# Kernel optimization log

Hardware: AMD Instinct MI355X
Metric: run time of the kernel (lower is better)

## Reference

```python
import jax, jax.numpy as jnp
import numpy as np

EPS = 1e-5
NUM_CRYSTALS = 64


def _bn(x2d, g, b):
    # torch BatchNorm1d in training mode: biased batch stats, affine
    m = x2d.mean(0)
    v = x2d.var(0)
    return g * (x2d - m) * jax.lax.rsqrt(v + EPS) + b


def _improved_conv(x, e, idx, p):
    (fcW, fcb, g1, b1, g2, b2, eW, eb, ge, be, W3, b3, g3, b3b) = p
    N, M = idx.shape
    A = x.shape[1]
    Bf = e.shape[2]
    xn = x[idx]  # (N, M, A) gathered neighbor atom features
    tot = jnp.concatenate([jnp.broadcast_to(x[:, None, :], (N, M, A)), xn, e], axis=2)  # (N,M,2A+B)
    # 2-body gated message
    h = jnp.einsum('nmf,of->nmo', tot, fcW) + fcb
    h = _bn(h.reshape(-1, 2 * A), g1, b1).reshape(N, M, 2 * A)
    two_body = jnp.sum(jax.nn.sigmoid(h[..., :A]) * jax.nn.softplus(h[..., A:]), axis=1)
    # explicit edge update
    he = jnp.einsum('nmf,of->nmo', tot, eW) + eb
    he = _bn(he.reshape(-1, 2 * Bf), ge, be).reshape(N, M, 2 * Bf)
    e_out = e + jax.nn.sigmoid(he[..., :Bf]) * jax.nn.softplus(he[..., Bf:])
    # 3-body: split W3 by concat blocks [x_i, x_j, x_l, e_ij, e_il] so the
    # (N,M,M,3A+2B) concat is never materialized; only (N,M,M,2A) is formed.
    Wa, Wj, Wl, Wij, Wil = jnp.split(W3, [A, 2 * A, 3 * A, 3 * A + Bf], axis=1)
    h3 = ((x @ Wa.T)[:, None, None, :]
          + (xn @ Wj.T)[:, :, None, :]
          + (xn @ Wl.T)[:, None, :, :]
          + (e @ Wij.T)[:, :, None, :]
          + (e @ Wil.T)[:, None, :, :]
          + b3)  # (N, M, M, 2A)
    h3 = _bn(h3.reshape(-1, 2 * A), g3, b3b).reshape(N, M, M, 2 * A)
    three_body = jnp.sum(jax.nn.sigmoid(h3[..., :A]) * jax.nn.softplus(h3[..., A:]), axis=(1, 2))
    total = _bn(two_body + three_body, g2, b2)
    return jax.nn.softplus(x + total), e_out


def setup_inputs() -> dict:
    key = jax.random.key(0)
    ks = jax.random.split(key, 12)
    N, M, OF, A, BF, H, NC = 2000, 12, 92, 64, 41, 128, 3
    f = lambda k, s: jax.random.normal(k, s, dtype=jnp.float32) * 0.05
    z = lambda s: jnp.zeros(s, jnp.float32)
    o = lambda s: jnp.ones(s, jnp.float32)
    return {
        'atom_fea': jax.random.normal(ks[0], (N, OF), dtype=jnp.float32),
        'nbr_fea': jax.random.normal(ks[1], (N, M, BF), dtype=jnp.float32),
        'nbr_fea_idx': jax.random.randint(ks[2], (N, M), 0, N),
        'site_seg': jnp.sort(jax.random.randint(ks[3], (N,), 0, NUM_CRYSTALS)),
        'emb_W': f(ks[4], (A, OF)), 'emb_b': z((A,)),
        'fcW': f(ks[5], (NC, 2 * A, 2 * A + BF)), 'fcb': z((NC, 2 * A)),
        'bn1_g': o((NC, 2 * A)), 'bn1_b': z((NC, 2 * A)),
        'bn2_g': o((NC, A)), 'bn2_b': z((NC, A)),
        'eW': f(ks[6], (NC, 2 * BF, 2 * A + BF)), 'eb': z((NC, 2 * BF)),
        'bne_g': o((NC, 2 * BF)), 'bne_b': z((NC, 2 * BF)),
        'W3': f(ks[7], (NC, 2 * A, 3 * A + 2 * BF)), 'b3': z((NC, 2 * A)),
        'bn3_g': o((NC, 2 * A)), 'bn3_b': z((NC, 2 * A)),
        'fc1W': f(ks[8], (H, A)), 'fc1b': z((H,)),
        'outW': f(ks[9], (1, H)), 'outb': z((1,)),
    }


def reference(atom_fea, nbr_fea, nbr_fea_idx, site_seg, emb_W, emb_b,
              fcW, fcb, bn1_g, bn1_b, bn2_g, bn2_b, eW, eb, bne_g, bne_b,
              W3, b3, bn3_g, bn3_b, fc1W, fc1b, outW, outb):
    x = atom_fea @ emb_W.T + emb_b  # embedding1 (orbital=False)
    e = nbr_fea
    n_conv = fcW.shape[0]
    for i in range(n_conv):  # small fixed layer loop
        p = (fcW[i], fcb[i], bn1_g[i], bn1_b[i], bn2_g[i], bn2_b[i],
             eW[i], eb[i], bne_g[i], bne_b[i], W3[i], b3[i], bn3_g[i], bn3_b[i])
        x, e = _improved_conv(x, e, nbr_fea_idx, p)
    x = jax.nn.softplus(jax.nn.softplus(x) @ fc1W.T + fc1b)  # conv_to_fc1
    # per-crystal mean pooling over site segments
    N = x.shape[0]
    sums = jax.ops.segment_sum(x, site_seg, num_segments=NUM_CRYSTALS)
    counts = jax.ops.segment_sum(jnp.ones((N, 1), x.dtype), site_seg, num_segments=NUM_CRYSTALS)
    pooled = sums / jnp.maximum(counts, 1.0)
    return pooled @ outW.T + outb  # (NUM_CRYSTALS, 1)
```

## Files before the change

### kernel.cpp

```cpp
#include <hip/hip_runtime.h>
#include <hip/hip_bf16.h>

#define N_ATOM 2000
#define MNBR   12
#define OFEA   92
#define AF     64
#define BFEA   41
#define K1     169
#define O1     128
#define OE     82
#define K3     274
#define NM     24000
#define NCONV  3
#define HID    128
#define NCRY   64
#define EPS_BN 1e-5f

#define LDA_T  192
#define LDH    512
#define LDSW   88
#define LDE    48

typedef __bf16 bf16x8 __attribute__((ext_vector_type(8)));
typedef float  f32x4  __attribute__((ext_vector_type(4)));

__device__ __forceinline__ float sigmoidf_(float x){
    return __builtin_amdgcn_rcpf(1.f + __expf(-x));
}
__device__ __forceinline__ float softplusf_(float x){
    return fmaxf(x,0.f) + __logf(1.f + __expf(-fabsf(x)));
}

__device__ __forceinline__ uint4 pack_bf16_8(const float* v){
    __hip_bfloat16 o[8];
    #pragma unroll
    for (int j=0;j<8;j++) o[j] = __float2bfloat16(v[j]);
    return *(const uint4*)o;
}

__global__ __launch_bounds__(256, 3)
void gemm_fused(const float* __restrict__ X,
                const float* __restrict__ E48,
                const int*   __restrict__ idx,
                const __hip_bfloat16* __restrict__ W,
                const float* __restrict__ bias,
                float* __restrict__ REST,
                float* __restrict__ STL,
                float* __restrict__ SPA,
                float* __restrict__ SQA)
{
    __shared__ unsigned short As[128][LDSW];
    __shared__ unsigned short Ws[128][LDSW];
    __shared__ float cs1[128];
    __shared__ float cs2[128];
    __shared__ float spa[12][128];

    const int tid  = threadIdx.x;
    const int row0 = blockIdx.x * 128;
    const int col0 = blockIdx.y * 128;
    const int w    = tid >> 6;
    const int l    = tid & 63;
    const int wm   = w >> 1, wn = w & 1;
    const int lrow = l & 15;
    const int quad = l >> 4;

    if (tid < 128){ cs1[tid] = 0.f; cs2[tid] = 0.f; }
    for (int ii = tid; ii < 12*128; ii += 256) spa[ii>>7][ii&127] = 0.f;

    f32x4 acc[4][4];
    #pragma unroll
    for (int i=0;i<4;i++)
        #pragma unroll
        for (int j=0;j<4;j++) acc[i][j] = (f32x4){0.f,0.f,0.f,0.f};

    #pragma unroll
    for (int it = 0; it < 3; ++it){
        const int k0 = it * 64;
        if (it) __syncthreads();
        #pragma unroll
        for (int j = 0; j < 4; ++j){
            int e  = tid + j*256;
            int r  = e >> 3;
            int kk = (e & 7) << 3;
            int grow = row0 + r;
            float v[8];
            #pragma unroll
            for (int q2=0;q2<8;q2++) v[q2] = 0.f;
            if (grow < NM){
                if (it == 2){
                    if (kk < LDE){
                        const float* s = E48 + (size_t)grow*LDE + kk;
                        float4 a0 = *(const float4*)s;
                        float4 a1 = *(const float4*)(s+4);
                        v[0]=a0.x; v[1]=a0.y; v[2]=a0.z; v[3]=a0.w;
                        v[4]=a1.x; v[5]=a1.y; v[6]=a1.z; v[7]=a1.w;
                    }
                } else {
                    const float* s = (it == 0)
                        ? X + (size_t)((unsigned)grow/12u)*AF + kk
                        : X + (size_t)idx[grow]*AF + kk;
                    float4 a0 = *(const float4*)s;
                    float4 a1 = *(const float4*)(s+4);
                    v[0]=a0.x; v[1]=a0.y; v[2]=a0.z; v[3]=a0.w;
                    v[4]=a1.x; v[5]=a1.y; v[6]=a1.z; v[7]=a1.w;
                }
            }
            *(uint4*)(&As[r][kk]) = pack_bf16_8(v);
            uint4 vw = *(const uint4*)(W + (size_t)(col0 + r)*LDA_T + k0 + kk);
            *(uint4*)(&Ws[r][kk]) = vw;
        }
        __syncthreads();
        #pragma unroll
        for (int ks = 0; ks < 2; ++ks){
            int koff = ks*32 + quad*8;
            bf16x8 a_[4], b_[4];
            #pragma unroll
            for (int mi=0;mi<4;mi++)
                a_[mi] = *(const bf16x8*)(&As[wm*64 + mi*16 + lrow][koff]);
            #pragma unroll
            for (int ni=0;ni<4;ni++)
                b_[ni] = *(const bf16x8*)(&Ws[wn*64 + ni*16 + lrow][koff]);
            #pragma unroll
            for (int mi=0;mi<4;mi++)
                #pragma unroll
                for (int ni=0;ni<4;ni++)
                    acc[mi][ni] = __builtin_amdgcn_mfma_f32_16x16x32_bf16(
                        a_[mi], b_[ni], acc[mi][ni], 0, 0, 0);
        }
    }

    const bool isPQ = (col0 >= 256);
    const int atomBase = (unsigned)row0 / 12u;
    int rbase_[4], n0_[4], sp_[4];
    #pragma unroll
    for (int mi=0;mi<4;mi++){
        rbase_[mi] = row0 + wm*64 + mi*16 + quad*4;
        int n0 = (int)((unsigned)rbase_[mi] / 12u);
        n0_[mi] = n0;
        sp_[mi] = 12 - (rbase_[mi] - n0*12);
    }

    #pragma unroll
    for (int ni=0;ni<4;ni++){
        const int cl  = wn*64 + ni*16 + lrow;
        const int col = col0 + cl;
        const float bv = bias[col];
        float s1 = 0.f, s2 = 0.f;
        #pragma unroll
        for (int mi=0;mi<4;mi++){
            const int rbase = rbase_[mi];
            float run0 = 0.f, run1 = 0.f;
            #pragma unroll
            for (int reg=0;reg<4;reg++){
                int grow = rbase + reg;
                if (grow < NM){
                    float vv = acc[mi][ni][reg] + bv;
                    if (col0 != 128 || col < 210)
                        REST[(size_t)grow*LDH + col] = vv;
                    s1 += vv; s2 += vv*vv;
                    if (isPQ){
                        if (reg < sp_[mi]) run0 += vv; else run1 += vv;
                    }
                }
            }
            if (isPQ){
                if (run0 != 0.f) atomicAdd(&spa[n0_[mi]     - atomBase][cl], run0);
                if (run1 != 0.f) atomicAdd(&spa[n0_[mi] + 1 - atomBase][cl], run1);
            }
        }
        if (isPQ){
            atomicAdd(&cs2[cl], s2);
        } else {
            atomicAdd(&cs1[cl], s1);
            atomicAdd(&cs2[cl], s2);
        }
    }
    __syncthreads();
    if (!isPQ){
        if (tid < 128){
            atomicAdd(&STL[col0 + tid],       cs1[tid]);
            atomicAdd(&STL[256 + col0 + tid], cs2[tid]);
        }
    } else {
        if (tid < 128)
            atomicAdd(&STL[(col0 == 256 ? 896 : 1024) + tid], cs2[tid]);
        float* SPQd = (col0 == 256) ? SPA : SQA;
        for (int ii = tid; ii < 12*128; ii += 256){
            int ai = ii >> 7, c2 = ii & 127;
            int na = atomBase + ai;
            float val = spa[ai][c2];
            if (val != 0.f && na < N_ATOM)
                atomicAdd(&SPQd[(size_t)na*128 + c2], val);
        }
    }
}

__global__ __launch_bounds__(256)
void bn3_pre(const float* __restrict__ SPA, const float* __restrict__ SQA,
             float* __restrict__ STL)
{
    const int c    = threadIdx.x & 127;
    const int half = threadIdx.x >> 7;
    float s1 = 0.f, sx = 0.f;
    for (int n = blockIdx.x*2 + half; n < N_ATOM; n += 64){
        float p = SPA[(size_t)n*128 + c];
        float q = SQA[(size_t)n*128 + c];
        s1 += p + q;
        sx += p * q;
    }
    atomicAdd(&STL[512 + c], 12.f*s1);
    atomicAdd(&STL[640 + c], 2.f*sx);
}

#define BM 64
#define BN 128
#define BK 32
template<int EPI, int SPIN>
__global__ __launch_bounds__(256)
void gemm_tn(const float* __restrict__ T, int ldt, int R,
             const float* __restrict__ W, int ldw, int K, int O,
             const float* __restrict__ bias,
             float* __restrict__ C, int ldc)
{
    __shared__ float Ts[BM][BK+1];
    __shared__ float Ws2[BN][BK+1];
    const int tid = threadIdx.x;
    const int row0 = blockIdx.x * BM;
    const int tx = tid % 16;
    const int ty = tid / 16;
    float acc[4][8];
    #pragma unroll
    for (int i=0;i<4;i++)
        #pragma unroll
        for (int j=0;j<8;j++) acc[i][j]=0.f;

    for (int k0 = 0; k0 < K; k0 += BK) {
        #pragma unroll
        for (int i=0;i<(BM*BK)/256;i++){
            int e = tid + i*256;
            int r = e / BK, k = e % BK;
            int gr = row0 + r, gk = k0 + k;
            float v = 0.f;
            if (gr < R && gk < K){
                v = T[(size_t)gr*ldt + gk];
                if (SPIN) v = softplusf_(v);
            }
            Ts[r][k] = v;
        }
        #pragma unroll
        for (int i=0;i<(BN*BK)/256;i++){
            int e = tid + i*256;
            int r = e / BK, k = e % BK;
            int gk = k0 + k;
            Ws2[r][k] = (r < O && gk < K) ? W[(size_t)r*ldw + gk] : 0.f;
        }
        __syncthreads();
        #pragma unroll
        for (int k=0;k<BK;k++){
            float a_[4], b_[8];
            #pragma unroll
            for (int i=0;i<4;i++) a_[i] = Ts[ty*4+i][k];
            #pragma unroll
            for (int j=0;j<8;j++) b_[j] = Ws2[tx + j*16][k];
            #pragma unroll
            for (int i=0;i<4;i++)
                #pragma unroll
                for (int j=0;j<8;j++)
                    acc[i][j] += a_[i]*b_[j];
        }
        __syncthreads();
    }
    #pragma unroll
    for (int i=0;i<4;i++){
        int gr = row0 + ty*4 + i;
        if (gr >= R) continue;
        #pragma unroll
        for (int j=0;j<8;j++){
            int gc = tx + j*16;
            if (gc >= O) continue;
            float v = acc[i][j] + (bias ? bias[gc] : 0.f);
            if (EPI==1) v = softplusf_(v);
            C[(size_t)gr*ldc + gc] = v;
        }
    }
}

__global__ void pack_all(const float* __restrict__ fcW, const float* __restrict__ eW,
                         const float* __restrict__ W3, const float* __restrict__ fcb,
                         const float* __restrict__ eb, const float* __restrict__ b3,
                         __hip_bfloat16* __restrict__ WALL, float* __restrict__ BIAS)
{
    int i = blockIdx.x*blockDim.x + threadIdx.x;
    const int nW = NCONV*512*LDA_T;
    if (i < nW){
        int l = i/(512*LDA_T), rem = i%(512*LDA_T);
        int c = rem/LDA_T, k = rem%LDA_T;
        float v = 0.f;
        if (c < O1){
            if (k < K1) v = fcW[((size_t)l*O1 + c)*K1 + k];
        } else if (c < O1+OE){
            if (k < K1) v = eW[((size_t)l*OE + (c-O1))*K1 + k];
        } else if (c >= 256 && c < 384){
            int o = c - 256;
            const float* W3l = W3 + (size_t)l*O1*K3;
            if (k < AF)                        v = 0.5f * W3l[(size_t)o*K3 + k];
            else if (k < 2*AF)                 v = W3l[(size_t)o*K3 + k];
            else if (k < K1)                   v = W3l[(size_t)o*K3 + 192 + (k-128)];
        } else if (c >= 384){
            int o = c - 384;
            const float* W3l = W3 + (size_t)l*O1*K3;
            if (k < AF)                        v = 0.5f * W3l[(size_t)o*K3 + k];
            else if (k < 2*AF)                 v = W3l[(size_t)o*K3 + k + AF];
            else if (k < K1)                   v = W3l[(size_t)o*K3 + 233 + (k-128)];
        }
        WALL[i] = __float2bfloat16(v);
    } else if (i < nW + NCONV*512){
        int m = i - nW;
        int l = m/512, c = m%512;
        float v = 0.f;
        if (c < O1)         v = fcb[l*O1 + c];
        else if (c < O1+OE) v = eb[l*OE + (c-O1)];
        else if (c >= 256)  v = 0.5f * b3[l*O1 + ((c-256)&127)];
        BIAS[m] = v;
    }
}

__global__ void e_init(const float* __restrict__ nbr, float* __restrict__ E48)
{
    int i = blockIdx.x*blockDim.x + threadIdx.x;
    if (i >= NM*LDE) return;
    int r = i / LDE, k = i % LDE;
    E48[i] = (k < BFEA) ? nbr[(size_t)r*BFEA + k] : 0.f;
}

__global__ void bn_fin_all(const float* __restrict__ STL,
                           const float* __restrict__ g1, const float* __restrict__ b1,
                           const float* __restrict__ ge, const float* __restrict__ be,
                           const float* __restrict__ g3, const float* __restrict__ b3b,
                           float* __restrict__ SC)
{
    int c = threadIdx.x;
    const float* S1A = STL;
    const float* S2A = STL + 256;
    const float* S13 = STL + 512;
    const float* S23 = STL + 640;
    const float* S2P = STL + 896;
    const float* S2Q = STL + 1024;
    if (c < O1+OE){
        float mean = S1A[c]*(1.f/NM);
        float var  = fmaxf(S2A[c]*(1.f/NM) - mean*mean, 0.f);
        float gg = (c < O1) ? g1[c] : ge[c-O1];
        float bb = (c < O1) ? b1[c] : be[c-O1];
        float sc = gg * rsqrtf(var + EPS_BN);
        SC[c] = sc; SC[256+c] = bb - sc*mean;
    }
    if (c < O1){
        float inv  = 1.f/((float)NM*MNBR);
        float mean = S13[c]*inv;
        float ex2  = (S23[c] + 12.f*(S2P[c] + S2Q[c]))*inv;
        float var  = fmaxf(ex2 - mean*mean, 0.f);
        float sc = g3[c] * rsqrtf(var + EPS_BN);
        SC[512+c] = sc; SC[640+c] = b3b[c] - sc*mean;
    }
}

__global__ __launch_bounds__(128)
void consumer_k(const float* __restrict__ REST, const float* __restrict__ SC,
                float* __restrict__ TB, float* __restrict__ E48)
{
    __shared__ float red[128];
    const int n = blockIdx.x;
    const int t = threadIdx.x;
    const int a = t & 63;
    const int g = t >> 6;
    const float* base = REST + (size_t)n*MNBR*LDH;

    float sha = SC[a],      tha = SC[256+a];
    float shb = SC[64+a],   thb = SC[256+64+a];
    float s3lo = SC[512+a], s3hi = SC[512+64+a];
    float t3lo = SC[640+a], t3hi = SC[640+64+a];

    float Qa[MNBR], Qb[MNBR];
    #pragma unroll
    for (int m=0;m<MNBR;m++){
        const float* row = base + (size_t)m*LDH;
        Qa[m] = s3lo*row[384+a];
        Qb[m] = s3hi*row[448+a];
    }
    float acc = 0.f;
    #pragma unroll
    for (int j=0;j<6;j++){
        const float* row = base + (size_t)(g*6+j)*LDH;
        acc += sigmoidf_(sha*row[a]+tha) * softplusf_(shb*row[64+a]+thb);
        float ua = s3lo*row[256+a] + t3lo;
        float ub = s3hi*row[320+a] + t3hi;
        #pragma unroll
        for (int l2=0;l2<MNBR;l2++)
            acc += sigmoidf_(ua + Qa[l2]) * softplusf_(ub + Qb[l2]);
    }
    red[t] = acc;
    __syncthreads();
    if (g == 0)
        TB[(size_t)n*AF + a] = red[a] + red[64+a];
    for (int idx = t; idx < MNBR*BFEA; idx += 128){
        int m = idx / BFEA, b = idx % BFEA;
        const float* row = base + (size_t)m*LDH;
        float u = SC[O1+b]*row[O1+b]   + SC[256+O1+b];
        float v = SC[169+b]*row[169+b] + SC[256+169+b];
        E48[((size_t)n*MNBR + m)*LDE + b] += sigmoidf_(u) * softplusf_(v);
    }
}

__global__ __launch_bounds__(64)
void tb_stats_k(const float* __restrict__ TB,
                float* __restrict__ S1, float* __restrict__ S2)
{
    int t = threadIdx.x;
    float s1 = 0.f, s2 = 0.f;
    for (int r = blockIdx.x; r < N_ATOM; r += gridDim.x){
        float v = TB[(size_t)r*AF + t];
        s1 += v; s2 += v*v;
    }
    atomicAdd(&S1[t], s1);
    atomicAdd(&S2[t], s2);
}

__global__ void x_update_k(float* __restrict__ X, const float* __restrict__ TB,
                           const float* __restrict__ S12, const float* __restrict__ S22,
                           const float* __restrict__ g2, const float* __restrict__ b2,
                           int total)
{
    int i = blockIdx.x*blockDim.x + threadIdx.x;
    if (i >= total) return;
    int a = i & (AF-1);
    float mean = S12[a]*(1.f/N_ATOM);
    float var  = fmaxf(S22[a]*(1.f/N_ATOM) - mean*mean, 0.f);
    float sc = g2[a]*rsqrtf(var + EPS_BN);
    X[i] = softplusf_(X[i] + sc*TB[i] + (b2[a] - sc*mean));
}

__global__ __launch_bounds__(128)
void pool_out_k(const float* __restrict__ Z, const int* __restrict__ seg,
                const float* __restrict__ outW, const float* __restrict__ outb,
                float* __restrict__ out)
{
    __shared__ float red[128];
    const int c = blockIdx.x;
    const int h = threadIdx.x;
    int l0, l1;
    {
        int l=0, r=N_ATOM;
        while (l<r){ int m=(l+r)>>1; if (seg[m] < c) l=m+1; else r=m; }
        l0 = l;
        l=l0; r=N_ATOM;
        while (l<r){ int m=(l+r)>>1; if (seg[m] < c+1) l=m+1; else r=m; }
        l1 = l;
    }
    float s = 0.f;
    for (int n = l0; n < l1; ++n) s += Z[(size_t)n*HID + h];
    float cnt = fmaxf((float)(l1-l0), 1.f);
    red[h] = (s/cnt) * outW[h];
    __syncthreads();
    for (int off=64; off>0; off>>=1){
        if (h < off) red[h] += red[h+off];
        __syncthreads();
    }
    if (h == 0) out[c] = red[0] + outb[0];
}

extern "C" void kernel_launch(void* const* d_in, const int* in_sizes, int n_in,
                              void* d_out, int out_size, void* d_ws, size_t ws_size,
                              hipStream_t stream)
{
    const float* atom_fea = (const float*)d_in[0];
    const float* nbr_fea  = (const float*)d_in[1];
    const int*   nbr_idx  = (const int*)d_in[2];
    const int*   site_seg = (const int*)d_in[3];
    const float* emb_W = (const float*)d_in[4];
    const float* emb_b = (const float*)d_in[5];
    const float* fcW   = (const float*)d_in[6];
    const float* fcb   = (const float*)d_in[7];
    const float* bn1_g = (const float*)d_in[8];
    const float* bn1_b = (const float*)d_in[9];
    const float* bn2_g = (const float*)d_in[10];
    const float* bn2_b = (const float*)d_in[11];
    const float* eW    = (const float*)d_in[12];
    const float* eb    = (const float*)d_in[13];
    const float* bne_g = (const float*)d_in[14];
    const float* bne_b = (const float*)d_in[15];
    const float* W3    = (const float*)d_in[16];
    const float* b3    = (const float*)d_in[17];
    const float* bn3_g = (const float*)d_in[18];
    const float* bn3_b = (const float*)d_in[19];
    const float* fc1W  = (const float*)d_in[20];
    const float* fc1b  = (const float*)d_in[21];
    const float* outW  = (const float*)d_in[22];
    const float* outb  = (const float*)d_in[23];

    float* ws   = (float*)d_ws;
    float* X    = ws;
    float* E48  = ws + 128000;
    float* REST = ws + 1280000;
    float* TB   = ws + 13568000;
    float* Z    = ws + 13696000;
    float* ST   = ws + 13952000;
    float* SC   = ws + 13958144;
    float* SPQ  = ws + 13959168;
    __hip_bfloat16* WALL = (__hip_bfloat16*)(ws + 15495168);
    float* BIAS = ws + 15642624;

    {
        int tot = NCONV*512*LDA_T + NCONV*512;
        pack_all<<<(tot+255)/256, 256, 0, stream>>>(fcW, eW, W3, fcb, eb, b3, WALL, BIAS);
    }
    hipMemsetAsync(ST, 0, (size_t)(6144 + 1024 + 1536000) * sizeof(float), stream);
    gemm_tn<0,0><<<(N_ATOM+BM-1)/BM, 256, 0, stream>>>(atom_fea, OFEA, N_ATOM,
                                                       emb_W, OFEA, OFEA, AF, emb_b, X, AF);
    e_init<<<(NM*LDE+255)/256, 256, 0, stream>>>(nbr_fea, E48);

    for (int i = 0; i < NCONV; i++){
        const float* g1 = bn1_g + i*O1, *b1 = bn1_b + i*O1;
        const float* g2 = bn2_g + i*AF, *b2 = bn2_b + i*AF;
        const float* ge = bne_g + i*OE, *be = bne_b + i*OE;
        const float* g3 = bn3_g + i*O1, *b3b = bn3_b + i*O1;
        float* STL = ST + i*2048;
        float* SPA = SPQ + (size_t)i*512000;
        float* SQA = SPA + 256000;
        float *S12 = STL+768, *S22 = STL+832;

        {
            dim3 g((NM+127)/128, 4);
            gemm_fused<<<g, 256, 0, stream>>>(X, E48, nbr_idx,
                                              WALL + (size_t)i*512*LDA_T,
                                              BIAS + i*512, REST, STL, SPA, SQA);
        }
        bn3_pre<<<32, 256, 0, stream>>>(SPA, SQA, STL);
        bn_fin_all<<<1, 256, 0, stream>>>(STL, g1, b1, ge, be, g3, b3b, SC);
        consumer_k<<<N_ATOM, 128, 0, stream>>>(REST, SC, TB, E48);
        tb_stats_k<<<128, 64, 0, stream>>>(TB, S12, S22);
        x_update_k<<<(N_ATOM*AF+255)/256, 256, 0, stream>>>(X, TB, S12, S22, g2, b2,
                                                            N_ATOM*AF);
    }

    gemm_tn<1,1><<<(N_ATOM+BM-1)/BM, 256, 0, stream>>>(X, AF, N_ATOM, fc1W, AF, AF, HID,
                                                       fc1b, Z, HID);
    pool_out_k<<<NCRY, 128, 0, stream>>>(Z, site_seg, outW, outb, (float*)d_out);
}
```

Baseline: 405.3 us.

## Fuse each conv layer into one persistent kernel with grid barriers

Replaces the per-layer chain of gemm_fused, bn3_pre, bn_fin_all, consumer_k, tb_stats_k and x_update_k with a single persistent kernel of 250 blocks of 512 threads. Each block owns 8 atoms (96 edge rows) and all 512 output columns, and keeps the GEMM results in registers and LDS instead of writing the large REST buffer to global memory. Batch-norm statistics are combined across blocks through global atomics and two software grid barriers. This removes heavy global traffic and several launches, but it relies on all 250 blocks being co-resident, and it recomputes the 3-body pair terms per block with less parallelism per atom.

```diff
diff --git a/kernel.cpp b/kernel.cpp
--- a/kernel.cpp
+++ b/kernel.cpp
@@ -9,7 +9,6 @@
 #define K1     169
 #define O1     128
 #define OE     82
-#define K3     274
 #define NM     24000
 #define NCONV  3
 #define HID    128
@@ -17,199 +16,316 @@
 #define EPS_BN 1e-5f
 
 #define LDA_T  192
-#define LDH    512
 #define LDSW   88
 #define LDE    48
+#define LDP    260
+#define TPB    512
+#define NBLK   250
 
 typedef __bf16 bf16x8 __attribute__((ext_vector_type(8)));
 typedef float  f32x4  __attribute__((ext_vector_type(4)));
 
+#define AS_OFF    0
+#define WS_OFF    16896
+#define HPQ_OFF   16896
+#define BL_OFF    116736
+#define SCT_OFF   118784
+#define SHT_OFF   119808
+#define SC3_OFF   120832
+#define SH3_OFF   121344
+#define S13_OFF   121856
+#define S23_OFF   122368
+#define TBL_OFF   122880
+#define DYN_LDS   124928
+
 __device__ __forceinline__ float sigmoidf_(float x){
     return __builtin_amdgcn_rcpf(1.f + __expf(-x));
 }
 __device__ __forceinline__ float softplusf_(float x){
     return fmaxf(x,0.f) + __logf(1.f + __expf(-fabsf(x)));
 }
-
 __device__ __forceinline__ uint4 pack_bf16_8(const float* v){
     __hip_bfloat16 o[8];
     #pragma unroll
     for (int j=0;j<8;j++) o[j] = __float2bfloat16(v[j]);
     return *(const uint4*)o;
 }
-
-__global__ __launch_bounds__(256, 3)
-void gemm_fused(const float* __restrict__ X,
-                const float* __restrict__ E48,
-                const int*   __restrict__ idx,
-                const __hip_bfloat16* __restrict__ W,
-                const float* __restrict__ bias,
-                float* __restrict__ REST,
-                float* __restrict__ STL,
-                float* __restrict__ SPA,
-                float* __restrict__ SQA)
+__device__ __forceinline__ float aloadf(const float* p){
+    return __hip_atomic_load((float*)p, __ATOMIC_RELAXED, __HIP_MEMORY_SCOPE_AGENT);
+}
+
+__device__ __forceinline__ void gridbar(unsigned* bar, unsigned target){
+    __syncthreads();
+    if (threadIdx.x == 0){
+        unsigned* cnt = bar;
+        unsigned* gen = bar + 1;
+        unsigned g = __hip_atomic_load(gen, __ATOMIC_RELAXED, __HIP_MEMORY_SCOPE_AGENT);
+        unsigned a = __hip_atomic_fetch_add(cnt, 1u, __ATOMIC_ACQ_REL, __HIP_MEMORY_SCOPE_AGENT);
+        if (a + 1 == target){
+            __hip_atomic_store(cnt, 0u, __ATOMIC_RELAXED, __HIP_MEMORY_SCOPE_AGENT);
+            __hip_atomic_fetch_add(gen, 1u, __ATOMIC_RELEASE, __HIP_MEMORY_SCOPE_AGENT);
+        } else {
+            while (__hip_atomic_load(gen, __ATOMIC_ACQUIRE, __HIP_MEMORY_SCOPE_AGENT) == g)
+                __builtin_amdgcn_s_sleep(4);
+        }
+    }
+    __syncthreads();
+}
+
+__global__ __launch_bounds__(TPB, 2)
+void mega_k(float* __restrict__ X, float* __restrict__ E48,
+            const int* __restrict__ idx,
+            const __hip_bfloat16* __restrict__ W, const float* __restrict__ bias,
+            float* __restrict__ STL, unsigned* __restrict__ bar,
+            const float* __restrict__ g1, const float* __restrict__ b1,
+            const float* __restrict__ ge, const float* __restrict__ be,
+            const float* __restrict__ g3, const float* __restrict__ b3b,
+            const float* __restrict__ g2, const float* __restrict__ b2)
 {
-    __shared__ unsigned short As[128][LDSW];
-    __shared__ unsigned short Ws[128][LDSW];
-    __shared__ float cs1[128];
-    __shared__ float cs2[128];
-    __shared__ float spa[12][128];
-
-    const int tid  = threadIdx.x;
-    const int row0 = blockIdx.x * 128;
-    const int col0 = blockIdx.y * 128;
+    extern __shared__ char smem[];
+    unsigned short (*As)[LDSW] = (unsigned short(*)[LDSW])(smem + AS_OFF);
+    unsigned short (*Ws)[LDSW] = (unsigned short(*)[LDSW])(smem + WS_OFF);
+    float (*HPQ)[LDP] = (float(*)[LDP])(smem + HPQ_OFF);
+    float* bL   = (float*)(smem + BL_OFF);
+    float* scT  = (float*)(smem + SCT_OFF);
+    float* shT  = (float*)(smem + SHT_OFF);
+    float* sc3  = (float*)(smem + SC3_OFF);
+    float* sh3  = (float*)(smem + SH3_OFF);
+    float* s13L = (float*)(smem + S13_OFF);
+    float* s23L = (float*)(smem + S23_OFF);
+    float* tbL  = (float*)(smem + TBL_OFF);
+
+    const int tid = threadIdx.x;
     const int w    = tid >> 6;
     const int l    = tid & 63;
-    const int wm   = w >> 1, wn = w & 1;
+    const int wm   = w >> 2;
+    const int cg   = w & 3;
     const int lrow = l & 15;
     const int quad = l >> 4;
-
-    if (tid < 128){ cs1[tid] = 0.f; cs2[tid] = 0.f; }
-    for (int ii = tid; ii < 12*128; ii += 256) spa[ii>>7][ii&127] = 0.f;
-
-    f32x4 acc[4][4];
+    const int row0 = blockIdx.x * 96;
+    const int atomBase = blockIdx.x * 8;
+
+    bL[tid] = bias[tid];
+    if (tid < 128){ s13L[tid] = 0.f; s23L[tid] = 0.f; }
+
+    f32x4 acc[3][8];
     #pragma unroll
-    for (int i=0;i<4;i++)
-        #pragma unroll
-        for (int j=0;j<4;j++) acc[i][j] = (f32x4){0.f,0.f,0.f,0.f};
+    for (int i=0;i<3;i++)
+        #pragma unroll
+        for (int j=0;j<8;j++) acc[i][j] = (f32x4){0.f,0.f,0.f,0.f};
 
     #pragma unroll
     for (int it = 0; it < 3; ++it){
         const int k0 = it * 64;
-        if (it) __syncthreads();
-        #pragma unroll
-        for (int j = 0; j < 4; ++j){
-            int e  = tid + j*256;
+        __syncthreads();
+        for (int e = tid; e < 768; e += TPB){
             int r  = e >> 3;
             int kk = (e & 7) << 3;
             int grow = row0 + r;
             float v[8];
             #pragma unroll
             for (int q2=0;q2<8;q2++) v[q2] = 0.f;
-            if (grow < NM){
-                if (it == 2){
-                    if (kk < LDE){
-                        const float* s = E48 + (size_t)grow*LDE + kk;
-                        float4 a0 = *(const float4*)s;
-                        float4 a1 = *(const float4*)(s+4);
-                        v[0]=a0.x; v[1]=a0.y; v[2]=a0.z; v[3]=a0.w;
-                        v[4]=a1.x; v[5]=a1.y; v[6]=a1.z; v[7]=a1.w;
-                    }
-                } else {
-                    const float* s = (it == 0)
-                        ? X + (size_t)((unsigned)grow/12u)*AF + kk
-                        : X + (size_t)idx[grow]*AF + kk;
+            if (it == 2){
+                if (kk < LDE){
+                    const float* s = E48 + (size_t)grow*LDE + kk;
                     float4 a0 = *(const float4*)s;
                     float4 a1 = *(const float4*)(s+4);
                     v[0]=a0.x; v[1]=a0.y; v[2]=a0.z; v[3]=a0.w;
                     v[4]=a1.x; v[5]=a1.y; v[6]=a1.z; v[7]=a1.w;
                 }
+            } else {
+                const float* s = (it == 0)
+                    ? X + (size_t)(atomBase + r/12)*AF + kk
+                    : X + (size_t)idx[grow]*AF + kk;
+                float4 a0 = *(const float4*)s;
+                float4 a1 = *(const float4*)(s+4);
+                v[0]=a0.x; v[1]=a0.y; v[2]=a0.z; v[3]=a0.w;
+                v[4]=a1.x; v[5]=a1.y; v[6]=a1.z; v[7]=a1.w;
             }
             *(uint4*)(&As[r][kk]) = pack_bf16_8(v);
-            uint4 vw = *(const uint4*)(W + (size_t)(col0 + r)*LDA_T + k0 + kk);
-            *(uint4*)(&Ws[r][kk]) = vw;
+        }
+        for (int e = tid; e < 4096; e += TPB){
+            int r  = e >> 3;
+            int kk = (e & 7) << 3;
+            *(uint4*)(&Ws[r][kk]) = *(const uint4*)(W + (size_t)r*LDA_T + k0 + kk);
         }
         __syncthreads();
         #pragma unroll
         for (int ks = 0; ks < 2; ++ks){
             int koff = ks*32 + quad*8;
-            bf16x8 a_[4], b_[4];
-            #pragma unroll
-            for (int mi=0;mi<4;mi++)
-                a_[mi] = *(const bf16x8*)(&As[wm*64 + mi*16 + lrow][koff]);
-            #pragma unroll
-            for (int ni=0;ni<4;ni++)
-                b_[ni] = *(const bf16x8*)(&Ws[wn*64 + ni*16 + lrow][koff]);
-            #pragma unroll
-            for (int mi=0;mi<4;mi++)
+            bf16x8 a_[3], b_[8];
+            #pragma unroll
+            for (int mi=0;mi<3;mi++)
+                a_[mi] = *(const bf16x8*)(&As[wm*48 + mi*16 + lrow][koff]);
+            #pragma unroll
+            for (int ni=0;ni<8;ni++)
+                b_[ni] = *(const bf16x8*)(&Ws[cg*128 + ni*16 + lrow][koff]);
+            #pragma unroll
+            for (int mi=0;mi<3;mi++)
                 #pragma unroll
-                for (int ni=0;ni<4;ni++)
+                for (int ni=0;ni<8;ni++)
                     acc[mi][ni] = __builtin_amdgcn_mfma_f32_16x16x32_bf16(
                         a_[mi], b_[ni], acc[mi][ni], 0, 0, 0);
         }
     }
 
-    const bool isPQ = (col0 >= 256);
-    const int atomBase = (unsigned)row0 / 12u;
-    int rbase_[4], n0_[4], sp_[4];
-    #pragma unroll
-    for (int mi=0;mi<4;mi++){
-        rbase_[mi] = row0 + wm*64 + mi*16 + quad*4;
-        int n0 = (int)((unsigned)rbase_[mi] / 12u);
-        n0_[mi] = n0;
-        sp_[mi] = 12 - (rbase_[mi] - n0*12);
-    }
-
-    #pragma unroll
-    for (int ni=0;ni<4;ni++){
-        const int cl  = wn*64 + ni*16 + lrow;
-        const int col = col0 + cl;
-        const float bv = bias[col];
-        float s1 = 0.f, s2 = 0.f;
-        #pragma unroll
-        for (int mi=0;mi<4;mi++){
-            const int rbase = rbase_[mi];
-            float run0 = 0.f, run1 = 0.f;
-            #pragma unroll
-            for (int reg=0;reg<4;reg++){
-                int grow = rbase + reg;
-                if (grow < NM){
-                    float vv = acc[mi][ni][reg] + bv;
-                    if (col0 != 128 || col < 210)
-                        REST[(size_t)grow*LDH + col] = vv;
-                    s1 += vv; s2 += vv*vv;
-                    if (isPQ){
-                        if (reg < sp_[mi]) run0 += vv; else run1 += vv;
-                    }
+    __syncthreads();
+    if (cg < 2){
+        #pragma unroll
+        for (int mi=0;mi<3;mi++)
+            #pragma unroll
+            for (int ni=0;ni<8;ni++){
+                int cl = cg*128 + ni*16 + lrow;
+                float bv = bL[cl];
+                #pragma unroll
+                for (int reg=0;reg<4;reg++){
+                    int rl = wm*48 + mi*16 + quad*4 + reg;
+                    HPQ[rl][cl] = acc[mi][ni][reg] + bv;
                 }
             }
-            if (isPQ){
-                if (run0 != 0.f) atomicAdd(&spa[n0_[mi]     - atomBase][cl], run0);
-                if (run1 != 0.f) atomicAdd(&spa[n0_[mi] + 1 - atomBase][cl], run1);
+    }
+    __syncthreads();
+    if (tid < 256){
+        float s1 = 0.f, s2 = 0.f;
+        for (int r = 0; r < 96; ++r){
+            float v = HPQ[r][tid];
+            s1 += v; s2 += v*v;
+        }
+        atomicAdd(&STL[tid],       s1);
+        atomicAdd(&STL[256 + tid], s2);
+    }
+    __syncthreads();
+    if (cg >= 2){
+        #pragma unroll
+        for (int mi=0;mi<3;mi++)
+            #pragma unroll
+            for (int ni=0;ni<8;ni++){
+                int cl = (cg-2)*128 + ni*16 + lrow;
+                float bv = bL[256 + cl];
+                #pragma unroll
+                for (int reg=0;reg<4;reg++){
+                    int rl = wm*48 + mi*16 + quad*4 + reg;
+                    HPQ[rl][cl] = acc[mi][ni][reg] + bv;
+                }
             }
-        }
-        if (isPQ){
-            atomicAdd(&cs2[cl], s2);
-        } else {
-            atomicAdd(&cs1[cl], s1);
-            atomicAdd(&cs2[cl], s2);
-        }
-    }
-    __syncthreads();
-    if (!isPQ){
-        if (tid < 128){
-            atomicAdd(&STL[col0 + tid],       cs1[tid]);
-            atomicAdd(&STL[256 + col0 + tid], cs2[tid]);
-        }
-    } else {
-        if (tid < 128)
-            atomicAdd(&STL[(col0 == 256 ? 896 : 1024) + tid], cs2[tid]);
-        float* SPQd = (col0 == 256) ? SPA : SQA;
-        for (int ii = tid; ii < 12*128; ii += 256){
-            int ai = ii >> 7, c2 = ii & 127;
-            int na = atomBase + ai;
-            float val = spa[ai][c2];
-            if (val != 0.f && na < N_ATOM)
-                atomicAdd(&SPQd[(size_t)na*128 + c2], val);
-        }
-    }
-}
-
-__global__ __launch_bounds__(256)
-void bn3_pre(const float* __restrict__ SPA, const float* __restrict__ SQA,
-             float* __restrict__ STL)
-{
-    const int c    = threadIdx.x & 127;
-    const int half = threadIdx.x >> 7;
-    float s1 = 0.f, sx = 0.f;
-    for (int n = blockIdx.x*2 + half; n < N_ATOM; n += 64){
-        float p = SPA[(size_t)n*128 + c];
-        float q = SQA[(size_t)n*128 + c];
-        s1 += p + q;
-        sx += p * q;
-    }
-    atomicAdd(&STL[512 + c], 12.f*s1);
-    atomicAdd(&STL[640 + c], 2.f*sx);
+    }
+    __syncthreads();
+    for (int item = tid; item < 1024; item += TPB){
+        int n = item >> 7, c = item & 127;
+        int r0 = n * MNBR;
+        float sp=0.f, spp=0.f, sq=0.f, sqq=0.f;
+        #pragma unroll
+        for (int m=0;m<MNBR;m++){
+            float p = HPQ[r0+m][c];
+            float q = HPQ[r0+m][128+c];
+            sp += p; spp += p*p; sq += q; sqq += q*q;
+        }
+        atomicAdd(&s13L[c], 12.f*(sp+sq));
+        atomicAdd(&s23L[c], 12.f*(spp+sqq) + 2.f*sp*sq);
+    }
+    __syncthreads();
+    if (tid < 128){
+        atomicAdd(&STL[512 + tid], s13L[tid]);
+        atomicAdd(&STL[640 + tid], s23L[tid]);
+    }
+
+    gridbar(bar, NBLK);
+
+    if (tid < 256){
+        int c = tid;
+        if (c < O1+OE){
+            float mean = aloadf(&STL[c]) * (1.f/NM);
+            float var  = fmaxf(aloadf(&STL[256+c])*(1.f/NM) - mean*mean, 0.f);
+            float gg = (c < O1) ? g1[c] : ge[c-O1];
+            float bb = (c < O1) ? b1[c] : be[c-O1];
+            float sc = gg * rsqrtf(var + EPS_BN);
+            scT[c] = sc; shT[c] = bb - sc*mean;
+        }
+    } else if (tid < 384){
+        int c = tid - 256;
+        float inv  = 1.f/((float)NM*MNBR);
+        float mean = aloadf(&STL[512+c]) * inv;
+        float var  = fmaxf(aloadf(&STL[640+c])*inv - mean*mean, 0.f);
+        float sc = g3[c] * rsqrtf(var + EPS_BN);
+        sc3[c] = sc; sh3[c] = b3b[c] - sc*mean;
+    }
+    __syncthreads();
+
+    const int r0a = w * MNBR;
+    float acc3 = 0.f;
+    {
+        float s3lo = sc3[l],    t3lo = sh3[l];
+        float s3hi = sc3[64+l], t3hi = sh3[64+l];
+        float Qa[MNBR], Qb[MNBR], ua[MNBR], ub[MNBR];
+        #pragma unroll
+        for (int m=0;m<MNBR;m++){
+            Qa[m] = s3lo*HPQ[r0a+m][128+l];
+            Qb[m] = s3hi*HPQ[r0a+m][192+l];
+            ua[m] = s3lo*HPQ[r0a+m][l]      + t3lo;
+            ub[m] = s3hi*HPQ[r0a+m][64+l]   + t3hi;
+        }
+        #pragma unroll
+        for (int m=0;m<MNBR;m++)
+            #pragma unroll
+            for (int l2=0;l2<MNBR;l2++)
+                acc3 += sigmoidf_(ua[m]+Qa[l2]) * softplusf_(ub[m]+Qb[l2]);
+    }
+    __syncthreads();
+    if (cg < 2){
+        #pragma unroll
+        for (int mi=0;mi<3;mi++)
+            #pragma unroll
+            for (int ni=0;ni<8;ni++){
+                int cl = cg*128 + ni*16 + lrow;
+                float bv = bL[cl];
+                #pragma unroll
+                for (int reg=0;reg<4;reg++){
+                    int rl = wm*48 + mi*16 + quad*4 + reg;
+                    HPQ[rl][cl] = acc[mi][ni][reg] + bv;
+                }
+            }
+    }
+    __syncthreads();
+    {
+        float sha = scT[l],    tha = shT[l];
+        float shb = scT[64+l], thb = shT[64+l];
+        float acc2 = 0.f;
+        #pragma unroll
+        for (int m=0;m<MNBR;m++)
+            acc2 += sigmoidf_(sha*HPQ[r0a+m][l]+tha) * softplusf_(shb*HPQ[r0a+m][64+l]+thb);
+        tbL[tid] = acc2 + acc3;
+    }
+    for (int item = tid; item < 8*MNBR*BFEA; item += TPB){
+        int n = item / (MNBR*BFEA);
+        int rem = item % (MNBR*BFEA);
+        int m = rem / BFEA, b = rem % BFEA;
+        const float* hr = HPQ[n*MNBR + m];
+        float u = scT[O1+b]*hr[O1+b]   + shT[O1+b];
+        float vv = scT[169+b]*hr[169+b] + shT[169+b];
+        E48[((size_t)(atomBase+n)*MNBR + m)*LDE + b] += sigmoidf_(u) * softplusf_(vv);
+    }
+    __syncthreads();
+    if (tid < 64){
+        float s1 = 0.f, s2 = 0.f;
+        #pragma unroll
+        for (int n=0;n<8;n++){
+            float v = tbL[n*64 + tid];
+            s1 += v; s2 += v*v;
+        }
+        atomicAdd(&STL[768 + tid], s1);
+        atomicAdd(&STL[832 + tid], s2);
+    }
+
+    gridbar(bar, NBLK);
+
+    {
+        int n = tid >> 6, a2 = tid & 63;
+        float mean = aloadf(&STL[768+a2]) * (1.f/N_ATOM);
+        float var  = fmaxf(aloadf(&STL[832+a2])*(1.f/N_ATOM) - mean*mean, 0.f);
+        float sc = g2[a2]*rsqrtf(var + EPS_BN);
+        size_t gx = (size_t)(atomBase+n)*AF + a2;
+        X[gx] = softplusf_(X[gx] + sc*tbL[tid] + (b2[a2] - sc*mean));
+    }
 }
 
 #define BM 64
@@ -293,34 +409,34 @@
     int i = blockIdx.x*blockDim.x + threadIdx.x;
     const int nW = NCONV*512*LDA_T;
     if (i < nW){
-        int l = i/(512*LDA_T), rem = i%(512*LDA_T);
+        int ll = i/(512*LDA_T), rem = i%(512*LDA_T);
         int c = rem/LDA_T, k = rem%LDA_T;
         float v = 0.f;
         if (c < O1){
-            if (k < K1) v = fcW[((size_t)l*O1 + c)*K1 + k];
+            if (k < K1) v = fcW[((size_t)ll*O1 + c)*K1 + k];
         } else if (c < O1+OE){
-            if (k < K1) v = eW[((size_t)l*OE + (c-O1))*K1 + k];
+            if (k < K1) v = eW[((size_t)ll*OE + (c-O1))*K1 + k];
         } else if (c >= 256 && c < 384){
             int o = c - 256;
-            const float* W3l = W3 + (size_t)l*O1*K3;
-            if (k < AF)                        v = 0.5f * W3l[(size_t)o*K3 + k];
-            else if (k < 2*AF)                 v = W3l[(size_t)o*K3 + k];
-            else if (k < K1)                   v = W3l[(size_t)o*K3 + 192 + (k-128)];
+            const float* W3l = W3 + (size_t)ll*O1*274;
+            if (k < AF)                        v = 0.5f * W3l[(size_t)o*274 + k];
+            else if (k < 2*AF)                 v = W3l[(size_t)o*274 + k];
+            else if (k < K1)                   v = W3l[(size_t)o*274 + 192 + (k-128)];
         } else if (c >= 384){
             int o = c - 384;
-            const float* W3l = W3 + (size_t)l*O1*K3;
-            if (k < AF)                        v = 0.5f * W3l[(size_t)o*K3 + k];
-            else if (k < 2*AF)                 v = W3l[(size_t)o*K3 + k + AF];
-            else if (k < K1)                   v = W3l[(size_t)o*K3 + 233 + (k-128)];
+            const float* W3l = W3 + (size_t)ll*O1*274;
+            if (k < AF)                        v = 0.5f * W3l[(size_t)o*274 + k];
+            else if (k < 2*AF)                 v = W3l[(size_t)o*274 + k + AF];
+            else if (k < K1)                   v = W3l[(size_t)o*274 + 233 + (k-128)];
         }
         WALL[i] = __float2bfloat16(v);
     } else if (i < nW + NCONV*512){
         int m = i - nW;
-        int l = m/512, c = m%512;
+        int ll = m/512, c = m%512;
         float v = 0.f;
-        if (c < O1)         v = fcb[l*O1 + c];
-        else if (c < O1+OE) v = eb[l*OE + (c-O1)];
-        else if (c >= 256)  v = 0.5f * b3[l*O1 + ((c-256)&127)];
+        if (c < O1)         v = fcb[ll*O1 + c];
+        else if (c < O1+OE) v = eb[ll*OE + (c-O1)];
+        else if (c >= 256)  v = 0.5f * b3[ll*O1 + ((c-256)&127)];
         BIAS[m] = v;
     }
 }
@@ -331,112 +447,6 @@
     if (i >= NM*LDE) return;
     int r = i / LDE, k = i % LDE;
     E48[i] = (k < BFEA) ? nbr[(size_t)r*BFEA + k] : 0.f;
-}
-
-__global__ void bn_fin_all(const float* __restrict__ STL,
-                           const float* __restrict__ g1, const float* __restrict__ b1,
-                           const float* __restrict__ ge, const float* __restrict__ be,
-                           const float* __restrict__ g3, const float* __restrict__ b3b,
-                           float* __restrict__ SC)
-{
-    int c = threadIdx.x;
-    const float* S1A = STL;
-    const float* S2A = STL + 256;
-    const float* S13 = STL + 512;
-    const float* S23 = STL + 640;
-    const float* S2P = STL + 896;
-    const float* S2Q = STL + 1024;
-    if (c < O1+OE){
-        float mean = S1A[c]*(1.f/NM);
-        float var  = fmaxf(S2A[c]*(1.f/NM) - mean*mean, 0.f);
-        float gg = (c < O1) ? g1[c] : ge[c-O1];
-        float bb = (c < O1) ? b1[c] : be[c-O1];
-        float sc = gg * rsqrtf(var + EPS_BN);
-        SC[c] = sc; SC[256+c] = bb - sc*mean;
-    }
-    if (c < O1){
-        float inv  = 1.f/((float)NM*MNBR);
-        float mean = S13[c]*inv;
-        float ex2  = (S23[c] + 12.f*(S2P[c] + S2Q[c]))*inv;
-        float var  = fmaxf(ex2 - mean*mean, 0.f);
-        float sc = g3[c] * rsqrtf(var + EPS_BN);
-        SC[512+c] = sc; SC[640+c] = b3b[c] - sc*mean;
-    }
-}
-
-__global__ __launch_bounds__(128)
-void consumer_k(const float* __restrict__ REST, const float* __restrict__ SC,
-                float* __restrict__ TB, float* __restrict__ E48)
-{
-    __shared__ float red[128];
-    const int n = blockIdx.x;
-    const int t = threadIdx.x;
-    const int a = t & 63;
-    const int g = t >> 6;
-    const float* base = REST + (size_t)n*MNBR*LDH;
-
-    float sha = SC[a],      tha = SC[256+a];
-    float shb = SC[64+a],   thb = SC[256+64+a];
-    float s3lo = SC[512+a], s3hi = SC[512+64+a];
-    float t3lo = SC[640+a], t3hi = SC[640+64+a];
-
-    float Qa[MNBR], Qb[MNBR];
-    #pragma unroll
-    for (int m=0;m<MNBR;m++){
-        const float* row = base + (size_t)m*LDH;
-        Qa[m] = s3lo*row[384+a];
-        Qb[m] = s3hi*row[448+a];
-    }
-    float acc = 0.f;
-    #pragma unroll
-    for (int j=0;j<6;j++){
-        const float* row = base + (size_t)(g*6+j)*LDH;
-        acc += sigmoidf_(sha*row[a]+tha) * softplusf_(shb*row[64+a]+thb);
-        float ua = s3lo*row[256+a] + t3lo;
-        float ub = s3hi*row[320+a] + t3hi;
-        #pragma unroll
-        for (int l2=0;l2<MNBR;l2++)
-            acc += sigmoidf_(ua + Qa[l2]) * softplusf_(ub + Qb[l2]);
-    }
-    red[t] = acc;
-    __syncthreads();
-    if (g == 0)
-        TB[(size_t)n*AF + a] = red[a] + red[64+a];
-    for (int idx = t; idx < MNBR*BFEA; idx += 128){
-        int m = idx / BFEA, b = idx % BFEA;
-        const float* row = base + (size_t)m*LDH;
-        float u = SC[O1+b]*row[O1+b]   + SC[256+O1+b];
-        float v = SC[169+b]*row[169+b] + SC[256+169+b];
-        E48[((size_t)n*MNBR + m)*LDE + b] += sigmoidf_(u) * softplusf_(v);
-    }
-}
-
-__global__ __launch_bounds__(64)
-void tb_stats_k(const float* __restrict__ TB,
-                float* __restrict__ S1, float* __restrict__ S2)
-{
-    int t = threadIdx.x;
-    float s1 = 0.f, s2 = 0.f;
-    for (int r = blockIdx.x; r < N_ATOM; r += gridDim.x){
-        float v = TB[(size_t)r*AF + t];
-        s1 += v; s2 += v*v;
-    }
-    atomicAdd(&S1[t], s1);
-    atomicAdd(&S2[t], s2);
-}
-
-__global__ void x_update_k(float* __restrict__ X, const float* __restrict__ TB,
-                           const float* __restrict__ S12, const float* __restrict__ S22,
-                           const float* __restrict__ g2, const float* __restrict__ b2,
-                           int total)
-{
-    int i = blockIdx.x*blockDim.x + threadIdx.x;
-    if (i >= total) return;
-    int a = i & (AF-1);
-    float mean = S12[a]*(1.f/N_ATOM);
-    float var  = fmaxf(S22[a]*(1.f/N_ATOM) - mean*mean, 0.f);
-    float sc = g2[a]*rsqrtf(var + EPS_BN);
-    X[i] = softplusf_(X[i] + sc*TB[i] + (b2[a] - sc*mean));
 }
 
 __global__ __launch_bounds__(128)
@@ -500,46 +510,37 @@
     float* ws   = (float*)d_ws;
     float* X    = ws;
     float* E48  = ws + 128000;
-    float* REST = ws + 1280000;
-    float* TB   = ws + 13568000;
-    float* Z    = ws + 13696000;
-    float* ST   = ws + 13952000;
-    float* SC   = ws + 13958144;
-    float* SPQ  = ws + 13959168;
-    __hip_bfloat16* WALL = (__hip_bfloat16*)(ws + 15495168);
-    float* BIAS = ws + 15642624;
+    float* Z    = ws + 1280000;
+    float* ST   = ws + 1536000;
+    unsigned* BAR = (unsigned*)(ws + 1542144);
+    __hip_bfloat16* WALL = (__hip_bfloat16*)(ws + 1542160);
+    float* BIAS = ws + 1689616;
+
+    static int s_attr = 0;
+    if (!s_attr){
+        hipFuncSetAttribute((const void*)mega_k,
+                            hipFuncAttributeMaxDynamicSharedMemorySize, DYN_LDS);
+        s_attr = 1;
+    }
 
     {
         int tot = NCONV*512*LDA_T + NCONV*512;
         pack_all<<<(tot+255)/256, 256, 0, stream>>>(fcW, eW, W3, fcb, eb, b3, WALL, BIAS);
     }
-    hipMemsetAsync(ST, 0, (size_t)(6144 + 1024 + 1536000) * sizeof(float), stream);
+    hipMemsetAsync(ST, 0, (size_t)(6144 + 16) * sizeof(float), stream);
     gemm_tn<0,0><<<(N_ATOM+BM-1)/BM, 256, 0, stream>>>(atom_fea, OFEA, N_ATOM,
                                                        emb_W, OFEA, OFEA, AF, emb_b, X, AF);
     e_init<<<(NM*LDE+255)/256, 256, 0, stream>>>(nbr_fea, E48);
 
     for (int i = 0; i < NCONV; i++){
-        const float* g1 = bn1_g + i*O1, *b1 = bn1_b + i*O1;
-        const float* g2 = bn2_g + i*AF, *b2 = bn2_b + i*AF;
-        const float* ge = bne_g + i*OE, *be = bne_b + i*OE;
-        const float* g3 = bn3_g + i*O1, *b3b = bn3_b + i*O1;
-        float* STL = ST + i*2048;
-        float* SPA = SPQ + (size_t)i*512000;
-        float* SQA = SPA + 256000;
-        float *S12 = STL+768, *S22 = STL+832;
-
-        {
-            dim3 g((NM+127)/128, 4);
-            gemm_fused<<<g, 256, 0, stream>>>(X, E48, nbr_idx,
-                                              WALL + (size_t)i*512*LDA_T,
-                                              BIAS + i*512, REST, STL, SPA, SQA);
-        }
-        bn3_pre<<<32, 256, 0, stream>>>(SPA, SQA, STL);
-        bn_fin_all<<<1, 256, 0, stream>>>(STL, g1, b1, ge, be, g3, b3b, SC);
-        consumer_k<<<N_ATOM, 128, 0, stream>>>(REST, SC, TB, E48);
-        tb_stats_k<<<128, 64, 0, stream>>>(TB, S12, S22);
-        x_update_k<<<(N_ATOM*AF+255)/256, 256, 0, stream>>>(X, TB, S12, S22, g2, b2,
-                                                            N_ATOM*AF);
+        mega_k<<<NBLK, TPB, DYN_LDS, stream>>>(
+            X, E48, nbr_idx,
+            WALL + (size_t)i*512*LDA_T, BIAS + i*512,
+            ST + i*2048, BAR,
+            bn1_g + i*O1, bn1_b + i*O1,
+            bne_g + i*OE, bne_b + i*OE,
+            bn3_g + i*O1, bn3_b + i*O1,
+            bn2_g + i*AF, bn2_b + i*AF);
     }
 
     gemm_tn<1,1><<<(N_ATOM+BM-1)/BM, 256, 0, stream>>>(X, AF, N_ATOM, fc1W, AF, AF, HID,
```

Measured after the change: 1.044 ms. 2.58x slower.
